# Optimization experiments

Measured on AMD Instinct MI355X. Metric: run time of the kernel, lower is better.

## Reference

```python
import jax, jax.numpy as jnp
import numpy as np

N_NODES = 50000
N_EDGES = 800000
IN_DIM_N = 128
IN_DIM_E = 32
OUT_DIM = 128


def setup_inputs() -> dict:
    key = jax.random.key(0)
    k = jax.random.split(key, 6)
    nfeats = jax.random.normal(k[0], (N_NODES, IN_DIM_N), dtype=jnp.float32)
    efeats = jax.random.normal(k[1], (N_EDGES, IN_DIM_E), dtype=jnp.float32)
    # xavier-normal-ish scaling
    W_fc = jax.random.normal(k[2], (OUT_DIM, IN_DIM_N), dtype=jnp.float32) * (2.0 / np.sqrt(IN_DIM_N + OUT_DIM))
    W_attn = jax.random.normal(k[3], (1, 2 * OUT_DIM + IN_DIM_E), dtype=jnp.float32) * 0.08
    src = jax.random.randint(k[4], (N_EDGES,), 0, N_NODES, dtype=jnp.int32)
    dst = jax.random.randint(k[5], (N_EDGES,), 0, N_NODES, dtype=jnp.int32)
    return {"nfeats": nfeats, "efeats": efeats, "W_fc": W_fc, "W_attn": W_attn, "src": src, "dst": dst}


def reference(nfeats, efeats, W_fc, W_attn, src, dst):
    n_nodes = nfeats.shape[0]
    out_dim = W_fc.shape[0]
    in_dim_e = efeats.shape[1]

    # z = fc(nfeats)  [N, out_dim]
    z = nfeats @ W_fc.T

    # attn_fc(cat([z_src, efeats, z_dst])) split into three small dots
    a = W_attn[0]
    a_src = a[:out_dim]
    a_e = a[out_dim:out_dim + in_dim_e]
    a_dst = a[out_dim + in_dim_e:]
    s_src = z @ a_src            # [N]
    s_dst = z @ a_dst            # [N]
    s_e = efeats @ a_e           # [E]

    # per-edge attention logit + leaky_relu (torch default slope 0.01)
    e = jax.nn.leaky_relu(s_src[src] + s_e + s_dst[dst], negative_slope=0.01)  # [E]

    # segment softmax over incoming edges of each dst node
    m = jax.ops.segment_max(e, dst, num_segments=n_nodes)
    m = jnp.where(jnp.isfinite(m), m, 0.0)  # guard zero-degree nodes
    w = jnp.exp(e - m[dst])
    denom = jax.ops.segment_sum(w, dst, num_segments=n_nodes)
    alpha = w / jnp.where(denom > 0, denom, 1.0)[dst]  # [E]

    # weighted sum of source z into dst nodes
    h = jax.ops.segment_sum(alpha[:, None] * z[src], dst, num_segments=n_nodes)  # [N, out_dim]
    return h
```

## Files before the change

kernel.cpp:

```cpp
#include <hip/hip_runtime.h>
#include <math.h>

#define N_NODES 50000
#define N_EDGES 800000
#define IN_DIM_N 128
#define IN_DIM_E 32
#define OUT_DIM 128
#define SCAN_BLOCKS ((N_NODES + 255) / 256)

__device__ inline unsigned bf16_rne(float x) {
    unsigned u = __float_as_uint(x);
    return (u + 0x7FFFu + ((u >> 16) & 1u)) >> 16;
}
__device__ inline unsigned pack_bf2(float a, float b) {
    return bf16_rne(a) | (bf16_rne(b) << 16);
}

__global__ void transpose_w_kernel(const float* __restrict__ W, float* __restrict__ Wt) {
    int i = blockIdx.x * 256 + threadIdx.x;
    if (i < 128 * 128) {
        int c = i >> 7, k = i & 127;
        Wt[k * 128 + c] = W[i];
    }
}

#define GEMM_ROWS 16
__launch_bounds__(256)
__global__ void gemm_kernel(const float* __restrict__ A, const float* __restrict__ Wt,
                            const float* __restrict__ attn,
                            unsigned* __restrict__ zb, float* __restrict__ s_src,
                            float* __restrict__ s_dst) {
    __shared__ float Wl[128 * 132];
    __shared__ float Al[GEMM_ROWS * 128];
    __shared__ float asrc[128], adst[128];
    int tid = threadIdx.x;

    for (int i = tid; i < 128 * 32; i += 256) {
        int k = i >> 5, q = i & 31;
        float4 v = ((const float4*)Wt)[k * 32 + q];
        *((float4*)&Wl[k * 132 + q * 4]) = v;
    }
    if (tid < 128) { asrc[tid] = attn[tid]; adst[tid] = attn[160 + tid]; }

    int row0 = blockIdx.x * GEMM_ROWS;
    for (int i = tid; i < GEMM_ROWS * 32; i += 256) {
        int r = i >> 5, q = i & 31;
        int gr = row0 + r;
        float4 v = make_float4(0.f, 0.f, 0.f, 0.f);
        if (gr < N_NODES) v = ((const float4*)A)[gr * 32 + q];
        *((float4*)&Al[r * 128 + q * 4]) = v;
    }
    __syncthreads();

    int lane_c = (tid & 31) * 4;
    int r_local = tid >> 5;
    const float* A0 = &Al[r_local * 128];
    const float* A1 = &Al[(r_local + 8) * 128];
    float4 acc0 = make_float4(0.f, 0.f, 0.f, 0.f);
    float4 acc1 = make_float4(0.f, 0.f, 0.f, 0.f);

    for (int k = 0; k < 128; ++k) {
        float4 wv = *((const float4*)&Wl[k * 132 + lane_c]);
        float a0 = A0[k], a1 = A1[k];
        acc0.x = fmaf(a0, wv.x, acc0.x); acc0.y = fmaf(a0, wv.y, acc0.y);
        acc0.z = fmaf(a0, wv.z, acc0.z); acc0.w = fmaf(a0, wv.w, acc0.w);
        acc1.x = fmaf(a1, wv.x, acc1.x); acc1.y = fmaf(a1, wv.y, acc1.y);
        acc1.z = fmaf(a1, wv.z, acc1.z); acc1.w = fmaf(a1, wv.w, acc1.w);
    }

    int gr0 = row0 + r_local, gr1 = row0 + r_local + 8;
    if (gr0 < N_NODES) {
        uint2 p = make_uint2(pack_bf2(acc0.x, acc0.y), pack_bf2(acc0.z, acc0.w));
        ((uint2*)zb)[(long)gr0 * 32 + (tid & 31)] = p;
    }
    if (gr1 < N_NODES) {
        uint2 p = make_uint2(pack_bf2(acc1.x, acc1.y), pack_bf2(acc1.z, acc1.w));
        ((uint2*)zb)[(long)gr1 * 32 + (tid & 31)] = p;
    }

    float4 as = *((float4*)&asrc[lane_c]);
    float4 ad = *((float4*)&adst[lane_c]);
    float ps0 = acc0.x * as.x + acc0.y * as.y + acc0.z * as.z + acc0.w * as.w;
    float pd0 = acc0.x * ad.x + acc0.y * ad.y + acc0.z * ad.z + acc0.w * ad.w;
    float ps1 = acc1.x * as.x + acc1.y * as.y + acc1.z * as.z + acc1.w * as.w;
    float pd1 = acc1.x * ad.x + acc1.y * ad.y + acc1.z * ad.z + acc1.w * ad.w;
    for (int off = 16; off; off >>= 1) {
        ps0 += __shfl_down(ps0, off, 32);
        pd0 += __shfl_down(pd0, off, 32);
        ps1 += __shfl_down(ps1, off, 32);
        pd1 += __shfl_down(pd1, off, 32);
    }
    if ((tid & 31) == 0) {
        if (gr0 < N_NODES) { s_src[gr0] = ps0; s_dst[gr0] = pd0; }
        if (gr1 < N_NODES) { s_src[gr1] = ps1; s_dst[gr1] = pd1; }
    }
}

__global__ void edge_score_hist_kernel(const float* __restrict__ efeats, const float* __restrict__ attn,
                                       const int* __restrict__ src, const int* __restrict__ dst,
                                       const float* __restrict__ s_src, const float* __restrict__ s_dst,
                                       int* __restrict__ counts, unsigned short* __restrict__ ranks,
                                       unsigned short* __restrict__ wq) {
    int i = blockIdx.x * blockDim.x + threadIdx.x;
    if (i >= N_EDGES) return;
    const float4* ef = (const float4*)(efeats + (long)i * IN_DIM_E);
    const float4* ae = (const float4*)(attn + OUT_DIM);
    float se = 0.f;
#pragma unroll
    for (int q = 0; q < IN_DIM_E / 4; ++q) {
        float4 v = ef[q];
        float4 a = ae[q];
        se += v.x * a.x + v.y * a.y + v.z * a.z + v.w * a.w;
    }
    int s = src[i], d = dst[i];
    float x = s_src[s] + se + s_dst[d];
    float ev = (x >= 0.f) ? x : 0.01f * x;
    float w = expf(ev);
    wq[i] = (unsigned short)bf16_rne(w);
    ranks[i] = (unsigned short)atomicAdd(&counts[d], 1);
}

__launch_bounds__(256)
__global__ void scan1_kernel(const int* __restrict__ counts, int* __restrict__ offsets,
                             int* __restrict__ blocksums) {
    int i = blockIdx.x * 256 + threadIdx.x;
    int v = (i < N_NODES) ? counts[i] : 0;
    int lane = threadIdx.x & 63;
    int wv = threadIdx.x >> 6;
    int x = v;
    for (int off = 1; off < 64; off <<= 1) {
        int y = __shfl_up(x, off, 64);
        if (lane >= off) x += y;
    }
    __shared__ int wsum[4];
    if (lane == 63) wsum[wv] = x;
    __syncthreads();
    int base = 0;
    for (int w = 0; w < wv; ++w) base += wsum[w];
    if (i < N_NODES) offsets[i] = base + x - v;
    if (threadIdx.x == 255) blocksums[blockIdx.x] = base + x;
}

__launch_bounds__(256)
__global__ void scan2_kernel(int* __restrict__ blocksums) {
    int t = threadIdx.x;
    int v = (t < SCAN_BLOCKS) ? blocksums[t] : 0;
    int lane = t & 63;
    int wv = t >> 6;
    int x = v;
    for (int off = 1; off < 64; off <<= 1) {
        int y = __shfl_up(x, off, 64);
        if (lane >= off) x += y;
    }
    __shared__ int wsum[4];
    if (lane == 63) wsum[wv] = x;
    __syncthreads();
    int base = 0;
    for (int w = 0; w < wv; ++w) base += wsum[w];
    if (t < SCAN_BLOCKS) blocksums[t] = base + x - v;
}

__launch_bounds__(256)
__global__ void scan3_kernel(int* __restrict__ offsets, const int* __restrict__ blocksums) {
    int i = blockIdx.x * 256 + threadIdx.x;
    if (i < N_NODES) offsets[i] += blocksums[blockIdx.x];
    if (i == 0) offsets[N_NODES] = N_EDGES;
}

__global__ void scatter_kernel(const int* __restrict__ src, const int* __restrict__ dst,
                               const unsigned short* __restrict__ ranks,
                               const unsigned short* __restrict__ wq,
                               const int* __restrict__ offsets, unsigned* __restrict__ pairs4) {
    int i = blockIdx.x * blockDim.x + threadIdx.x;
    if (i >= N_EDGES) return;
    int d = dst[i];
    int pos = offsets[d] + (int)ranks[i];
    pairs4[pos] = (unsigned)src[i] | ((unsigned)wq[i] << 16);
}

__launch_bounds__(256)
__global__ void aggregate_kernel(const unsigned* __restrict__ pairs4, const int* __restrict__ offsets,
                                 const unsigned* __restrict__ zb, float* __restrict__ h) {
    int node = blockIdx.x * 4 + (threadIdx.x >> 6);
    if (node >= N_NODES) return;
    int lane = threadIdx.x & 63;
    int beg = offsets[node], end = offsets[node + 1];
    float accx0 = 0.f, accy0 = 0.f, accx1 = 0.f, accy1 = 0.f;
    float dsum = 0.f;
    for (int base = beg; base < end; base += 64) {
        int n = min(64, end - base);
        unsigned u = 0;
        if (lane < n) {
            u = pairs4[base + lane];
            dsum += __uint_as_float(u & 0xFFFF0000u);
        }
        int j = 0;
        for (; j + 1 < n; j += 2) {
            unsigned u0 = (unsigned)__shfl((int)u, j, 64);
            unsigned u1 = (unsigned)__shfl((int)u, j + 1, 64);
            unsigned z0 = zb[(long)(u0 & 0xFFFFu) * 64 + lane];
            unsigned z1 = zb[(long)(u1 & 0xFFFFu) * 64 + lane];
            float w0 = __uint_as_float(u0 & 0xFFFF0000u);
            float w1 = __uint_as_float(u1 & 0xFFFF0000u);
            accx0 = fmaf(w0, __uint_as_float(z0 << 16), accx0);
            accy0 = fmaf(w0, __uint_as_float(z0 & 0xFFFF0000u), accy0);
            accx1 = fmaf(w1, __uint_as_float(z1 << 16), accx1);
            accy1 = fmaf(w1, __uint_as_float(z1 & 0xFFFF0000u), accy1);
        }
        if (j < n) {
            unsigned u0 = (unsigned)__shfl((int)u, j, 64);
            unsigned z0 = zb[(long)(u0 & 0xFFFFu) * 64 + lane];
            float w0 = __uint_as_float(u0 & 0xFFFF0000u);
            accx0 = fmaf(w0, __uint_as_float(z0 << 16), accx0);
            accy0 = fmaf(w0, __uint_as_float(z0 & 0xFFFF0000u), accy0);
        }
    }
    float accx = accx0 + accx1, accy = accy0 + accy1;
    for (int off = 32; off; off >>= 1) dsum += __shfl_xor(dsum, off, 64);
    float scale = 1.f / (dsum > 0.f ? dsum : 1.f);
    ((float2*)h)[(long)node * 64 + lane] = make_float2(accx * scale, accy * scale);
}

extern "C" void kernel_launch(void* const* d_in, const int* in_sizes, int n_in,
                              void* d_out, int out_size, void* d_ws, size_t ws_size,
                              hipStream_t stream) {
    const float* nfeats = (const float*)d_in[0];
    const float* efeats = (const float*)d_in[1];
    const float* W_fc   = (const float*)d_in[2];
    const float* W_attn = (const float*)d_in[3];
    const int*   src    = (const int*)d_in[4];
    const int*   dst    = (const int*)d_in[5];
    float* h = (float*)d_out;

    char* ws = (char*)d_ws;
    unsigned* zb     = (unsigned*)ws;
    float* s_src     = (float*)(ws + (size_t)N_NODES * 64 * 4);
    float* s_dst     = s_src + N_NODES;
    float* Wt        = s_dst + N_NODES;
    int*   counts    = (int*)(Wt + 128 * 128);
    int*   offsets   = counts + N_NODES;
    int*   blocksums = offsets + N_NODES + 1;
    unsigned short* ranks = (unsigned short*)(blocksums + SCAN_BLOCKS + 4);
    unsigned short* wq    = ranks + N_EDGES;
    unsigned* pairs4      = (unsigned*)(wq + N_EDGES);

    hipMemsetAsync(counts, 0, N_NODES * sizeof(int), stream);
    transpose_w_kernel<<<64, 256, 0, stream>>>(W_fc, Wt);
    gemm_kernel<<<(N_NODES + GEMM_ROWS - 1) / GEMM_ROWS, 256, 0, stream>>>(
        nfeats, Wt, W_attn, zb, s_src, s_dst);
    edge_score_hist_kernel<<<(N_EDGES + 255) / 256, 256, 0, stream>>>(
        efeats, W_attn, src, dst, s_src, s_dst, counts, ranks, wq);
    scan1_kernel<<<SCAN_BLOCKS, 256, 0, stream>>>(counts, offsets, blocksums);
    scan2_kernel<<<1, 256, 0, stream>>>(blocksums);
    scan3_kernel<<<SCAN_BLOCKS, 256, 0, stream>>>(offsets, blocksums);
    scatter_kernel<<<(N_EDGES + 255) / 256, 256, 0, stream>>>(
        src, dst, ranks, wq, offsets, pairs4);
    aggregate_kernel<<<(N_NODES + 3) / 4, 256, 0, stream>>>(pairs4, offsets, zb, h);
}
```

Baseline: 305.4 us.

## Replace scalar FP32 node GEMM with bf16 MFMA GEMM using prepacked weight fragments

```diff
diff --git a/kernel.cpp b/kernel.cpp
--- a/kernel.cpp
+++ b/kernel.cpp
@@ -8,6 +8,9 @@
 #define OUT_DIM 128
 #define SCAN_BLOCKS ((N_NODES + 255) / 256)
 
+typedef __bf16 bf16x8 __attribute__((ext_vector_type(8)));
+typedef float  f32x4  __attribute__((ext_vector_type(4)));
+
 __device__ inline unsigned bf16_rne(float x) {
     unsigned u = __float_as_uint(x);
     return (u + 0x7FFFu + ((u >> 16) & 1u)) >> 16;
@@ -16,83 +19,98 @@
     return bf16_rne(a) | (bf16_rne(b) << 16);
 }
 
-__global__ void transpose_w_kernel(const float* __restrict__ W, float* __restrict__ Wt) {
-    int i = blockIdx.x * 256 + threadIdx.x;
-    if (i < 128 * 128) {
-        int c = i >> 7, k = i & 127;
-        Wt[k * 128 + c] = W[i];
-    }
-}
-
-#define GEMM_ROWS 16
-__launch_bounds__(256)
-__global__ void gemm_kernel(const float* __restrict__ A, const float* __restrict__ Wt,
-                            const float* __restrict__ attn,
-                            unsigned* __restrict__ zb, float* __restrict__ s_src,
-                            float* __restrict__ s_dst) {
-    __shared__ float Wl[128 * 132];
-    __shared__ float Al[GEMM_ROWS * 128];
+__global__ void wfrag_kernel(const float* __restrict__ W, unsigned* __restrict__ Wfrag) {
+    int t = blockIdx.x * 256 + threadIdx.x;
+    if (t >= 2048) return;
+    int lane = t & 63;
+    int tile = (t >> 6) & 7;
+    int ks   = t >> 9;
+    int n  = tile * 16 + (lane & 15);
+    int kb = ks * 32 + (lane >> 4) * 8;
+    const float* srcp = W + n * 128 + kb;
+    unsigned o[4];
+#pragma unroll
+    for (int j = 0; j < 4; ++j) o[j] = pack_bf2(srcp[2 * j], srcp[2 * j + 1]);
+    ((uint4*)Wfrag)[t] = *(uint4*)o;
+}
+
+__launch_bounds__(256)
+__global__ void gemm_mfma_kernel(const float* __restrict__ A, const unsigned* __restrict__ Wfrag,
+                                 const float* __restrict__ attn, unsigned* __restrict__ zb,
+                                 float* __restrict__ s_src, float* __restrict__ s_dst) {
+    __shared__ unsigned Au[64 * 68];
+    __shared__ unsigned Bu[8192];
     __shared__ float asrc[128], adst[128];
     int tid = threadIdx.x;
-
-    for (int i = tid; i < 128 * 32; i += 256) {
-        int k = i >> 5, q = i & 31;
-        float4 v = ((const float4*)Wt)[k * 32 + q];
-        *((float4*)&Wl[k * 132 + q * 4]) = v;
+    int row0 = blockIdx.x * 64;
+
+    {
+        const uint4* g = (const uint4*)Wfrag;
+        uint4* l = (uint4*)Bu;
+        for (int i = tid; i < 2048; i += 256) l[i] = g[i];
     }
     if (tid < 128) { asrc[tid] = attn[tid]; adst[tid] = attn[160 + tid]; }
 
-    int row0 = blockIdx.x * GEMM_ROWS;
-    for (int i = tid; i < GEMM_ROWS * 32; i += 256) {
+    for (int i = tid; i < 64 * 32; i += 256) {
         int r = i >> 5, q = i & 31;
         int gr = row0 + r;
         float4 v = make_float4(0.f, 0.f, 0.f, 0.f);
-        if (gr < N_NODES) v = ((const float4*)A)[gr * 32 + q];
-        *((float4*)&Al[r * 128 + q * 4]) = v;
+        if (gr < N_NODES) v = ((const float4*)A)[(long)gr * 32 + q];
+        uint2 p = make_uint2(pack_bf2(v.x, v.y), pack_bf2(v.z, v.w));
+        *((uint2*)&Au[r * 68 + q * 2]) = p;
     }
     __syncthreads();
 
-    int lane_c = (tid & 31) * 4;
-    int r_local = tid >> 5;
-    const float* A0 = &Al[r_local * 128];
-    const float* A1 = &Al[(r_local + 8) * 128];
-    float4 acc0 = make_float4(0.f, 0.f, 0.f, 0.f);
-    float4 acc1 = make_float4(0.f, 0.f, 0.f, 0.f);
-
-    for (int k = 0; k < 128; ++k) {
-        float4 wv = *((const float4*)&Wl[k * 132 + lane_c]);
-        float a0 = A0[k], a1 = A1[k];
-        acc0.x = fmaf(a0, wv.x, acc0.x); acc0.y = fmaf(a0, wv.y, acc0.y);
-        acc0.z = fmaf(a0, wv.z, acc0.z); acc0.w = fmaf(a0, wv.w, acc0.w);
-        acc1.x = fmaf(a1, wv.x, acc1.x); acc1.y = fmaf(a1, wv.y, acc1.y);
-        acc1.z = fmaf(a1, wv.z, acc1.z); acc1.w = fmaf(a1, wv.w, acc1.w);
-    }
-
-    int gr0 = row0 + r_local, gr1 = row0 + r_local + 8;
-    if (gr0 < N_NODES) {
-        uint2 p = make_uint2(pack_bf2(acc0.x, acc0.y), pack_bf2(acc0.z, acc0.w));
-        ((uint2*)zb)[(long)gr0 * 32 + (tid & 31)] = p;
-    }
-    if (gr1 < N_NODES) {
-        uint2 p = make_uint2(pack_bf2(acc1.x, acc1.y), pack_bf2(acc1.z, acc1.w));
-        ((uint2*)zb)[(long)gr1 * 32 + (tid & 31)] = p;
-    }
-
-    float4 as = *((float4*)&asrc[lane_c]);
-    float4 ad = *((float4*)&adst[lane_c]);
-    float ps0 = acc0.x * as.x + acc0.y * as.y + acc0.z * as.z + acc0.w * as.w;
-    float pd0 = acc0.x * ad.x + acc0.y * ad.y + acc0.z * ad.z + acc0.w * ad.w;
-    float ps1 = acc1.x * as.x + acc1.y * as.y + acc1.z * as.z + acc1.w * as.w;
-    float pd1 = acc1.x * ad.x + acc1.y * ad.y + acc1.z * ad.z + acc1.w * ad.w;
-    for (int off = 16; off; off >>= 1) {
-        ps0 += __shfl_down(ps0, off, 32);
-        pd0 += __shfl_down(pd0, off, 32);
-        ps1 += __shfl_down(ps1, off, 32);
-        pd1 += __shfl_down(pd1, off, 32);
-    }
-    if ((tid & 31) == 0) {
-        if (gr0 < N_NODES) { s_src[gr0] = ps0; s_dst[gr0] = pd0; }
-        if (gr1 < N_NODES) { s_src[gr1] = ps1; s_dst[gr1] = pd1; }
+    int lane = tid & 63;
+    int wave = tid >> 6;
+    int m = lane & 15, quad = lane >> 4;
+
+    f32x4 acc[8];
+#pragma unroll
+    for (int t = 0; t < 8; ++t) acc[t] = (f32x4){0.f, 0.f, 0.f, 0.f};
+
+#pragma unroll
+    for (int ks = 0; ks < 4; ++ks) {
+        uint4 au = *((const uint4*)&Au[(wave * 16 + m) * 68 + ks * 16 + quad * 4]);
+        bf16x8 af = *(bf16x8*)&au;
+#pragma unroll
+        for (int t = 0; t < 8; ++t) {
+            uint4 bu = *((const uint4*)&Bu[((ks * 8 + t) * 64 + lane) * 4]);
+            bf16x8 bf = *(bf16x8*)&bu;
+            acc[t] = __builtin_amdgcn_mfma_f32_16x16x32_bf16(af, bf, acc[t], 0, 0, 0);
+        }
+    }
+
+    float ps[4] = {0.f, 0.f, 0.f, 0.f}, pd[4] = {0.f, 0.f, 0.f, 0.f};
+#pragma unroll
+    for (int t = 0; t < 8; ++t) {
+        float as_ = asrc[t * 16 + m], ad_ = adst[t * 16 + m];
+#pragma unroll
+        for (int r = 0; r < 4; ++r) {
+            float v = acc[t][r];
+            ps[r] = fmaf(v, as_, ps[r]);
+            pd[r] = fmaf(v, ad_, pd[r]);
+            float vn = __shfl_xor(v, 1, 64);
+            if (!(m & 1)) {
+                int grow = row0 + wave * 16 + quad * 4 + r;
+                if (grow < N_NODES)
+                    zb[(long)grow * 64 + t * 8 + (m >> 1)] = pack_bf2(v, vn);
+            }
+        }
+    }
+#pragma unroll
+    for (int r = 0; r < 4; ++r) {
+        for (int off = 1; off < 16; off <<= 1) {
+            ps[r] += __shfl_xor(ps[r], off, 64);
+            pd[r] += __shfl_xor(pd[r], off, 64);
+        }
+    }
+    if (m == 0) {
+#pragma unroll
+        for (int r = 0; r < 4; ++r) {
+            int grow = row0 + wave * 16 + quad * 4 + r;
+            if (grow < N_NODES) { s_src[grow] = ps[r]; s_dst[grow] = pd[r]; }
+        }
     }
 }
 
@@ -236,8 +254,8 @@
     unsigned* zb     = (unsigned*)ws;
     float* s_src     = (float*)(ws + (size_t)N_NODES * 64 * 4);
     float* s_dst     = s_src + N_NODES;
-    float* Wt        = s_dst + N_NODES;
-    int*   counts    = (int*)(Wt + 128 * 128);
+    unsigned* Wfrag  = (unsigned*)(s_dst + N_NODES);
+    int*   counts    = (int*)(Wfrag + 8192);
     int*   offsets   = counts + N_NODES;
     int*   blocksums = offsets + N_NODES + 1;
     unsigned short* ranks = (unsigned short*)(blocksums + SCAN_BLOCKS + 4);
@@ -245,9 +263,9 @@
     unsigned* pairs4      = (unsigned*)(wq + N_EDGES);
 
     hipMemsetAsync(counts, 0, N_NODES * sizeof(int), stream);
-    transpose_w_kernel<<<64, 256, 0, stream>>>(W_fc, Wt);
-    gemm_kernel<<<(N_NODES + GEMM_ROWS - 1) / GEMM_ROWS, 256, 0, stream>>>(
-        nfeats, Wt, W_attn, zb, s_src, s_dst);
+    wfrag_kernel<<<8, 256, 0, stream>>>(W_fc, Wfrag);
+    gemm_mfma_kernel<<<(N_NODES + 63) / 64, 256, 0, stream>>>(
+        nfeats, Wfrag, W_attn, zb, s_src, s_dst);
     edge_score_hist_kernel<<<(N_EDGES + 255) / 256, 256, 0, stream>>>(
         efeats, W_attn, src, dst, s_src, s_dst, counts, ranks, wq);
     scan1_kernel<<<SCAN_BLOCKS, 256, 0, stream>>>(counts, offsets, blocksums);
```

Measured after the change: 273.3 us. 10.5% less time.
